# Kernel tuning notes

Measured on AMD Instinct MI355X. Metric: run time of the kernel, lower is better.

Reference implementation:

```python
import jax, jax.numpy as jnp
import numpy as np

EPS = 1e-12  # tf.math.l2_normalize epsilon

def _l2norm(a, axis):
    # tf.math.l2_normalize: a * rsqrt(max(sum(a^2), eps))
    sq = jnp.sum(a * a, axis=axis, keepdims=True)
    return a * jax.lax.rsqrt(jnp.maximum(sq, EPS))

def setup_inputs() -> dict:
    key = jax.random.key(0)
    k1, k2 = jax.random.split(key)
    B, D, N = 4096, 512, 5994
    x = jax.random.normal(k1, (B, D), dtype=jnp.float32)
    W = jax.random.normal(k2, (D, N), dtype=jnp.float32)
    return {"x": x, "W": W}

def reference(x, W):
    # Normalize x along feature dim (axis=-1 of x), W along axis=-1 (output_dim),
    # exactly as in the TF layer; the broadcast multiply + reduce over input_dim
    # is mathematically a matmul: out[b,n] = sum_d xn[b,d] * Wn[d,n].
    xn = _l2norm(x, axis=-1)          # (B, D)
    Wn = _l2norm(W, axis=-1)          # (D, N), normalized per input-dim row
    return jnp.einsum('bd,dn->bn', xn, Wn)  # (B, N)
```

## Files before the change

kernel.cpp:

```cpp
#include <hip/hip_runtime.h>
#include <hip/hip_bf16.h>

typedef __attribute__((ext_vector_type(8))) short short8;
typedef __attribute__((ext_vector_type(4))) float floatx4;

#define L2EPS 1e-12f

__device__ __forceinline__ unsigned short f2bf(float f) {
  union { float f; unsigned u; } c; c.f = f;
  unsigned u = c.u;
  unsigned r = (u + 0x7fffu + ((u >> 16) & 1u)) >> 16;
  return (unsigned short)r;
}

__device__ __forceinline__ void gload_lds16(const void* g, void* l) {
  __builtin_amdgcn_global_load_lds(
      (const __attribute__((address_space(1))) unsigned int*)g,
      (__attribute__((address_space(3))) unsigned int*)l,
      16, 0, 0);
}

__global__ __launch_bounds__(256) void wnorm_kernel(const float* __restrict__ W,
                                                    float* __restrict__ rnw, int N) {
  const int d = blockIdx.x;
  const float2* row2 = (const float2*)(W + (size_t)d * N);
  const int n2 = N >> 1;
  float s = 0.f;
  for (int i = threadIdx.x; i < n2; i += 256) {
    const float2 v = row2[i];
    s += v.x * v.x + v.y * v.y;
  }
  if (threadIdx.x == 0 && (N & 1)) {
    const float v = W[(size_t)d * N + (N - 1)];
    s += v * v;
  }
#pragma unroll
  for (int off = 32; off > 0; off >>= 1) s += __shfl_xor(s, off);
  __shared__ float red[4];
  if ((threadIdx.x & 63) == 0) red[threadIdx.x >> 6] = s;
  __syncthreads();
  if (threadIdx.x == 0) {
    const float t = red[0] + red[1] + red[2] + red[3];
    rnw[d] = rsqrtf(fmaxf(t, L2EPS));
  }
}

__global__ __launch_bounds__(256) void prep_kernel(const float* __restrict__ x,
                                                   const float* __restrict__ W,
                                                   const float* __restrict__ rnw,
                                                   unsigned short* __restrict__ xb,
                                                   unsigned short* __restrict__ BT,
                                                   int N, int nxb, int nwx) {
  const int bid = blockIdx.x;
  if (bid < nxb) {
    const int lane = threadIdx.x & 63;
    const int wave = threadIdx.x >> 6;
    const int row  = bid * 4 + wave;
    const float4* xr = (const float4*)(x + (size_t)row * 512);
    const float4 v0 = xr[lane * 2];
    const float4 v1 = xr[lane * 2 + 1];
    float s = v0.x*v0.x + v0.y*v0.y + v0.z*v0.z + v0.w*v0.w
            + v1.x*v1.x + v1.y*v1.y + v1.z*v1.z + v1.w*v1.w;
#pragma unroll
    for (int off = 32; off > 0; off >>= 1) s += __shfl_xor(s, off);
    const float r = rsqrtf(fmaxf(s, L2EPS));
    const float4 w0 = ((const float4*)rnw)[lane * 2];
    const float4 w1 = ((const float4*)rnw)[lane * 2 + 1];
    short8 o;
    o[0] = (short)f2bf(v0.x * r * w0.x); o[1] = (short)f2bf(v0.y * r * w0.y);
    o[2] = (short)f2bf(v0.z * r * w0.z); o[3] = (short)f2bf(v0.w * r * w0.w);
    o[4] = (short)f2bf(v1.x * r * w1.x); o[5] = (short)f2bf(v1.y * r * w1.y);
    o[6] = (short)f2bf(v1.z * r * w1.z); o[7] = (short)f2bf(v1.w * r * w1.w);
    *(short8*)(xb + (size_t)row * 512 + lane * 8) = o;
  } else {
    __shared__ unsigned short tile[32][33];
    const int wb = bid - nxb;
    const int n0 = (wb % nwx) * 32;
    const int d0 = (wb / nwx) * 32;
    const int tx = threadIdx.x & 31;
    const int ty = threadIdx.x >> 5;
#pragma unroll
    for (int i = 0; i < 4; ++i) {
      const int dl = ty + i * 8;
      const int n = n0 + tx;
      float v = 0.f;
      if (n < N) v = W[(size_t)(d0 + dl) * N + n];
      tile[tx][dl] = f2bf(v);
    }
    __syncthreads();
#pragma unroll
    for (int i = 0; i < 4; ++i) {
      const int nl = ty + i * 8;
      BT[(size_t)(n0 + nl) * 512 + d0 + tx] = tile[nl][tx];
    }
  }
}

#define NT 16

__global__ __launch_bounds__(256, 3) void gemm_kernel(
    const unsigned short* __restrict__ A,
    const unsigned short* __restrict__ BT,
    float* __restrict__ C,
    int N, int nbx, int nby) {
  __shared__ unsigned short As[3][128 * 32];
  __shared__ unsigned short Bs[3][128 * 32];

  const int tid  = threadIdx.x;
  const int l    = tid & 63;
  const int w    = tid >> 6;
  const int wr   = w >> 1;
  const int wc   = w & 1;

  const int grid = nbx * nby;
  const int bid  = blockIdx.x;
  int swz = bid;
  if ((grid & 7) == 0) swz = (bid & 7) * (grid >> 3) + (bid >> 3);
  const int bx = swz / nby;
  const int by = swz % nby;
  const int row0 = by * 128;
  const int col0 = bx * 128;

  floatx4 acc[4][4];
#pragma unroll
  for (int m = 0; m < 4; ++m)
#pragma unroll
    for (int n = 0; n < 4; ++n)
      acc[m][n] = (floatx4){0.f, 0.f, 0.f, 0.f};

  const int srow = tid >> 2;
  const int sch  = ((tid & 3) ^ ((tid >> 3) & 3)) * 8;
  const unsigned short* Ag = A  + (size_t)(row0 + srow) * 512 + sch;
  const unsigned short* Bg = BT + (size_t)(col0 + srow) * 512 + sch;
  const int ldst = srow * 32 + (tid & 3) * 8;

#define STAGE(t_) do { \
    gload_lds16(Ag + (t_) * 32,                    &As[(t_) % 3][ldst]); \
    gload_lds16(Ag + (size_t)64 * 512 + (t_) * 32, &As[(t_) % 3][ldst + 2048]); \
    gload_lds16(Bg + (t_) * 32,                    &Bs[(t_) % 3][ldst]); \
    gload_lds16(Bg + (size_t)64 * 512 + (t_) * 32, &Bs[(t_) % 3][ldst + 2048]); \
  } while (0)
#define CFENCE asm volatile("" ::: "memory")

  const int ln15 = l & 15;
  const int qs   = (((l >> 4) ^ ((ln15 >> 1) & 3))) * 8;
  const int ab   = (wr * 64 + ln15) * 32 + qs;
  const int bb   = (wc * 64 + ln15) * 32 + qs;

  STAGE(0); STAGE(1);
  asm volatile("s_waitcnt vmcnt(4)" ::: "memory");
  __builtin_amdgcn_s_barrier();
  CFENCE;

#pragma unroll
  for (int t = 0; t < NT; ++t) {
    const int b = t % 3;
    if (t + 2 < NT) STAGE(t + 2);
    CFENCE;
    short8 af[4], bf[4];
#pragma unroll
    for (int m = 0; m < 4; ++m) af[m] = *(const short8*)&As[b][ab + m * 512];
#pragma unroll
    for (int n = 0; n < 4; ++n) bf[n] = *(const short8*)&Bs[b][bb + n * 512];
    CFENCE;
    __builtin_amdgcn_s_setprio(1);
#pragma unroll
    for (int m = 0; m < 4; ++m)
#pragma unroll
      for (int n = 0; n < 4; ++n)
        acc[m][n] = __builtin_amdgcn_mfma_f32_16x16x32_bf16(af[m], bf[n], acc[m][n], 0, 0, 0);
    __builtin_amdgcn_s_setprio(0);
    CFENCE;
    if (t < NT - 2)       asm volatile("s_waitcnt vmcnt(4)" ::: "memory");
    else if (t == NT - 2) asm volatile("s_waitcnt vmcnt(0)" ::: "memory");
    if (t < NT - 1) {
      __builtin_amdgcn_s_barrier();
      CFENCE;
    }
  }

  const int rb = row0 + wr * 64 + (l >> 4) * 4;
  const int cb = col0 + wc * 64 + ln15;
#pragma unroll
  for (int m = 0; m < 4; ++m) {
#pragma unroll
    for (int r = 0; r < 4; ++r) {
      const size_t o = (size_t)(rb + m * 16 + r) * N + cb;
#pragma unroll
      for (int n = 0; n < 4; ++n) {
        if (cb + n * 16 < N) C[o + n * 16] = acc[m][n][r];
      }
    }
  }
#undef STAGE
#undef CFENCE
}

extern "C" void kernel_launch(void* const* d_in, const int* in_sizes, int n_in,
                              void* d_out, int out_size, void* d_ws, size_t ws_size,
                              hipStream_t stream) {
  const float* x = (const float*)d_in[0];
  const float* W = (const float*)d_in[1];
  float* out = (float*)d_out;

  const int D = 512;
  const int B = in_sizes[0] / D;
  const int N = in_sizes[1] / D;
  const int Npad = ((N + 127) / 128) * 128;

  char* ws = (char*)d_ws;
  unsigned short* xb  = (unsigned short*)ws;
  unsigned short* BTb = (unsigned short*)(ws + (size_t)B * D * 2);
  float* rnw = (float*)(ws + (size_t)B * D * 2 + (size_t)Npad * D * 2);

  const int nby = B / 128;
  const int nbx = Npad / 128;
  const int nxb = B / 4;
  const int nwx = Npad / 32;
  const int nwb = nwx * (D / 32);

  wnorm_kernel<<<D, 256, 0, stream>>>(W, rnw, N);
  prep_kernel<<<nxb + nwb, 256, 0, stream>>>(x, W, rnw, xb, BTb, N, nxb, nwx);
  gemm_kernel<<<nbx * nby, 256, 0, stream>>>(xb, BTb, out, N, nbx, nby);
}
```

Measured before the change: 62.51 us.

## Replace triple-buffered BK=32 GEMM pipeline with single-buffered BK=64 loop

The GEMM main loop drops the explicit 3-stage LDS ring with manual vmcnt waits and setprio. It now uses a single 128x64 tile per operand with __syncthreads before and after compute, halving the number of k-iterations, and raises the occupancy hint to 4 blocks per CU. The intent is to cut barrier and pipeline overhead and rely on more resident blocks to hide latency. The cost is that global loads within a block no longer overlap its own MFMA work.

After: 60.33 us. -3.5%, faster.

```diff
diff --git a/kernel.cpp b/kernel.cpp
--- a/kernel.cpp
+++ b/kernel.cpp
@@ -96,21 +96,19 @@
   }
 }
 
-#define NT 16
-
-__global__ __launch_bounds__(256, 3) void gemm_kernel(
+__global__ __launch_bounds__(256, 4) void gemm_kernel(
     const unsigned short* __restrict__ A,
     const unsigned short* __restrict__ BT,
     float* __restrict__ C,
     int N, int nbx, int nby) {
-  __shared__ unsigned short As[3][128 * 32];
-  __shared__ unsigned short Bs[3][128 * 32];
-
-  const int tid  = threadIdx.x;
-  const int l    = tid & 63;
-  const int w    = tid >> 6;
-  const int wr   = w >> 1;
-  const int wc   = w & 1;
+  __shared__ unsigned short As[128 * 64];
+  __shared__ unsigned short Bs[128 * 64];
+
+  const int tid = threadIdx.x;
+  const int l   = tid & 63;
+  const int w   = tid >> 6;
+  const int wr  = w >> 1;
+  const int wc  = w & 1;
 
   const int grid = nbx * nby;
   const int bid  = blockIdx.x;
@@ -128,58 +126,46 @@
     for (int n = 0; n < 4; ++n)
       acc[m][n] = (floatx4){0.f, 0.f, 0.f, 0.f};
 
-  const int srow = tid >> 2;
-  const int sch  = ((tid & 3) ^ ((tid >> 3) & 3)) * 8;
-  const unsigned short* Ag = A  + (size_t)(row0 + srow) * 512 + sch;
-  const unsigned short* Bg = BT + (size_t)(col0 + srow) * 512 + sch;
-  const int ldst = srow * 32 + (tid & 3) * 8;
-
-#define STAGE(t_) do { \
-    gload_lds16(Ag + (t_) * 32,                    &As[(t_) % 3][ldst]); \
-    gload_lds16(Ag + (size_t)64 * 512 + (t_) * 32, &As[(t_) % 3][ldst + 2048]); \
-    gload_lds16(Bg + (t_) * 32,                    &Bs[(t_) % 3][ldst]); \
-    gload_lds16(Bg + (size_t)64 * 512 + (t_) * 32, &Bs[(t_) % 3][ldst + 2048]); \
-  } while (0)
-#define CFENCE asm volatile("" ::: "memory")
+  const int srow = tid >> 3;
+  const int sch  = ((tid & 7) ^ (srow & 7)) * 8;
+  const unsigned short* Ap = A  + (size_t)(row0 + srow) * 512 + sch;
+  const unsigned short* Bp = BT + (size_t)(col0 + srow) * 512 + sch;
+  const int lo = tid * 8;
 
   const int ln15 = l & 15;
-  const int qs   = (((l >> 4) ^ ((ln15 >> 1) & 3))) * 8;
-  const int ab   = (wr * 64 + ln15) * 32 + qs;
-  const int bb   = (wc * 64 + ln15) * 32 + qs;
-
-  STAGE(0); STAGE(1);
-  asm volatile("s_waitcnt vmcnt(4)" ::: "memory");
-  __builtin_amdgcn_s_barrier();
-  CFENCE;
-
-#pragma unroll
-  for (int t = 0; t < NT; ++t) {
-    const int b = t % 3;
-    if (t + 2 < NT) STAGE(t + 2);
-    CFENCE;
-    short8 af[4], bf[4];
-#pragma unroll
-    for (int m = 0; m < 4; ++m) af[m] = *(const short8*)&As[b][ab + m * 512];
-#pragma unroll
-    for (int n = 0; n < 4; ++n) bf[n] = *(const short8*)&Bs[b][bb + n * 512];
-    CFENCE;
-    __builtin_amdgcn_s_setprio(1);
-#pragma unroll
-    for (int m = 0; m < 4; ++m)
-#pragma unroll
-      for (int n = 0; n < 4; ++n)
-        acc[m][n] = __builtin_amdgcn_mfma_f32_16x16x32_bf16(af[m], bf[n], acc[m][n], 0, 0, 0);
-    __builtin_amdgcn_s_setprio(0);
-    CFENCE;
-    if (t < NT - 2)       asm volatile("s_waitcnt vmcnt(4)" ::: "memory");
-    else if (t == NT - 2) asm volatile("s_waitcnt vmcnt(0)" ::: "memory");
-    if (t < NT - 1) {
-      __builtin_amdgcn_s_barrier();
-      CFENCE;
-    }
-  }
-
-  const int rb = row0 + wr * 64 + (l >> 4) * 4;
+  const int q4   = l >> 4;
+  const int e7   = ln15 & 7;
+  const int cs0  = ((q4) ^ e7) * 8;
+  const int cs1  = ((4 + q4) ^ e7) * 8;
+  const int aoff = (wr * 64 + ln15) * 64;
+  const int boff = (wc * 64 + ln15) * 64;
+
+  for (int t = 0; t < 8; ++t) {
+#pragma unroll
+    for (int i = 0; i < 4; ++i)
+      gload_lds16(Ap + (size_t)(i * 32) * 512 + t * 64, &As[i * 2048 + lo]);
+#pragma unroll
+    for (int i = 0; i < 4; ++i)
+      gload_lds16(Bp + (size_t)(i * 32) * 512 + t * 64, &Bs[i * 2048 + lo]);
+    __syncthreads();
+#pragma unroll
+    for (int ks = 0; ks < 2; ++ks) {
+      const int cs = ks ? cs1 : cs0;
+      short8 af[4], bf[4];
+#pragma unroll
+      for (int m = 0; m < 4; ++m) af[m] = *(const short8*)&As[aoff + m * 1024 + cs];
+#pragma unroll
+      for (int n = 0; n < 4; ++n) bf[n] = *(const short8*)&Bs[boff + n * 1024 + cs];
+#pragma unroll
+      for (int m = 0; m < 4; ++m)
+#pragma unroll
+        for (int n = 0; n < 4; ++n)
+          acc[m][n] = __builtin_amdgcn_mfma_f32_16x16x32_bf16(af[m], bf[n], acc[m][n], 0, 0, 0);
+    }
+    __syncthreads();
+  }
+
+  const int rb = row0 + wr * 64 + q4 * 4;
   const int cb = col0 + wc * 64 + ln15;
 #pragma unroll
   for (int m = 0; m < 4; ++m) {
@@ -192,8 +178,6 @@
       }
     }
   }
-#undef STAGE
-#undef CFENCE
 }
 
 extern "C" void kernel_launch(void* const* d_in, const int* in_sizes, int n_in,
```
